# Kernel optimization log

Hardware: AMD Instinct MI355X
Metric: run time of the kernel (lower is better)

## Reference

```python
import jax, jax.numpy as jnp
import numpy as np

VOCAB = 32000
EMBED = 256
HIDDEN = 512
BATCH = 32
MAXLEN = 128


def setup_inputs() -> dict:
    key = jax.random.key(0)
    ks = jax.random.split(key, 8)
    s = 0.02
    return {
        "text": jax.random.randint(ks[0], (BATCH, MAXLEN), 0, VOCAB, dtype=jnp.int64),
        "embed": jax.random.normal(ks[1], (VOCAB, EMBED), dtype=jnp.float32) * s,
        "W_ih": jax.random.normal(ks[2], (4 * HIDDEN, EMBED), dtype=jnp.float32) * s,
        "W_hh": jax.random.normal(ks[3], (4 * HIDDEN, HIDDEN), dtype=jnp.float32) * s,
        "b_ih": jax.random.normal(ks[4], (4 * HIDDEN,), dtype=jnp.float32) * s,
        "b_hh": jax.random.normal(ks[5], (4 * HIDDEN,), dtype=jnp.float32) * s,
        "W_fc": jax.random.normal(ks[6], (VOCAB, HIDDEN), dtype=jnp.float32) * s,
        "b_fc": jax.random.normal(ks[7], (VOCAB,), dtype=jnp.float32) * s,
    }


def reference(text, embed, W_ih, W_hh, b_ih, b_hh, W_fc, b_fc):
    B, T = text.shape
    H = W_hh.shape[1]

    def step(carry, _):
        h, c, tok = carry
        x = embed[tok]                                  # [B, E] gather
        gates = x @ W_ih.T + b_ih + h @ W_hh.T + b_hh   # [B, 4H]
        i, f, g, o = jnp.split(gates, 4, axis=-1)       # PyTorch LSTMCell gate order
        i = jax.nn.sigmoid(i)
        f = jax.nn.sigmoid(f)
        g = jnp.tanh(g)
        o = jax.nn.sigmoid(o)
        c = f * c + i * g
        h = o * jnp.tanh(c)
        logits = h @ W_fc.T + b_fc                      # [B, V]
        tok = jnp.argmax(logits, axis=1)                # greedy feedback
        return (h, c, tok), logits

    # initial prediction = zeros[B,1] -> argmax = token 0; hidden=None -> zeros
    init = (
        jnp.zeros((B, H), dtype=embed.dtype),
        jnp.zeros((B, H), dtype=embed.dtype),
        jnp.zeros((B,), dtype=jnp.int32),
    )
    _, logits = jax.lax.scan(step, init, None, length=T)  # [T, B, V]
    return jnp.transpose(logits, (1, 0, 2))               # [B, T, V]
```

## Files before the change

### kernel.cpp

```cpp
#include <hip/hip_runtime.h>
#include <hip/hip_bf16.h>
#include <math.h>

#define VOCAB  32000
#define EMBED  256
#define HIDDEN 512
#define BATCH  32
#define MAXLEN 128
#define NCAND  250

typedef __attribute__((ext_vector_type(8))) short bf16x8;
typedef __attribute__((ext_vector_type(8))) unsigned short ushort8;
typedef __attribute__((ext_vector_type(4))) float f32x4;

#define WS_C_OFF     0
#define WS_HHI_OFF   65536
#define WS_HLO_OFF   131072
#define WS_CAND_OFF  196608
#define WS_WHI_OFF   260608
#define WS_WLO_OFF   33028608
#define WS_ZERO_BYTES 196608

__device__ __forceinline__ unsigned int f32_ordered_key(float f) {
    unsigned int b = __float_as_uint(f);
    return (b & 0x80000000u) ? ~b : (b | 0x80000000u);
}
__device__ __forceinline__ unsigned short f2bf(float x) {
    __hip_bfloat16 h = __float2bfloat16(x);
    return *reinterpret_cast<unsigned short*>(&h);
}
__device__ __forceinline__ float bf2f(unsigned short u) {
    __hip_bfloat16 h = *reinterpret_cast<__hip_bfloat16*>(&u);
    return __bfloat162float(h);
}

__global__ __launch_bounds__(256) void split_w_kernel(
    const float* __restrict__ W, unsigned short* __restrict__ hi,
    unsigned short* __restrict__ lo, int n4)
{
    const int stride = gridDim.x * blockDim.x;
    for (int i = blockIdx.x * blockDim.x + threadIdx.x; i < n4; i += stride) {
        f32x4 w = ((const f32x4*)W)[i];
        ushort4 hv, lv;
        #pragma unroll
        for (int j = 0; j < 4; ++j) {
            float x = w[j];
            unsigned short hb = f2bf(x);
            ((unsigned short*)&hv)[j] = hb;
            ((unsigned short*)&lv)[j] = f2bf(x - bf2f(hb));
        }
        ((ushort4*)hi)[i] = hv;
        ((ushort4*)lo)[i] = lv;
    }
}

__global__ __launch_bounds__(256) void lstm_step_kernel(
    const float* __restrict__ embed,
    const float* __restrict__ W_ih, const float* __restrict__ W_hh,
    const float* __restrict__ b_ih, const float* __restrict__ b_hh,
    const unsigned long long* __restrict__ cand,
    const unsigned short* __restrict__ hhi_prev, const unsigned short* __restrict__ hlo_prev,
    unsigned short* __restrict__ hhi_next, unsigned short* __restrict__ hlo_next,
    float* __restrict__ c_buf, int t)
{
    __shared__ float x_t[EMBED][33];
    __shared__ float h_t[HIDDEN][33];
    __shared__ int   tok_s[BATCH];
    __shared__ unsigned long long credl[8][BATCH];
    __shared__ float part[2][4][BATCH][4];
    __shared__ float gate_s[2][4][BATCH];

    const int tid = threadIdx.x;

    if (t > 0) {
        const int rb = tid & 31, seg = tid >> 5;
        unsigned long long m = 0ull;
        for (int i = seg; i < NCAND; i += 8) {
            unsigned long long e = cand[(size_t)i * BATCH + rb];
            if (e > m) m = e;
        }
        credl[seg][rb] = m;
        __syncthreads();
        if (tid < BATCH) {
            unsigned long long mm = credl[0][tid];
            #pragma unroll
            for (int ss = 1; ss < 8; ++ss) if (credl[ss][tid] > mm) mm = credl[ss][tid];
            tok_s[tid] = (int)(~(unsigned int)(mm & 0xFFFFFFFFull));
        }
    } else {
        if (tid < BATCH) tok_s[tid] = 0;
    }
    __syncthreads();

    {
        const int sb = tid >> 3, slot = tid & 7;
        const float* er = embed + (size_t)tok_s[sb] * EMBED;
        #pragma unroll
        for (int i = 0; i < 8; ++i) {
            int e4 = i * 8 + slot;
            float4 v = ((const float4*)er)[e4];
            int e = e4 * 4;
            x_t[e + 0][sb] = v.x; x_t[e + 1][sb] = v.y;
            x_t[e + 2][sb] = v.z; x_t[e + 3][sb] = v.w;
        }
        const ushort8* hr = (const ushort8*)(hhi_prev + (size_t)sb * HIDDEN);
        const ushort8* lr = (const ushort8*)(hlo_prev + (size_t)sb * HIDDEN);
        #pragma unroll
        for (int i = 0; i < 8; ++i) {
            int u = i * 8 + slot;
            ushort8 hv = hr[u], lv = lr[u];
            #pragma unroll
            for (int e = 0; e < 8; ++e)
                h_t[u * 8 + e][sb] = bf2f((unsigned short)hv[e]) + bf2f((unsigned short)lv[e]);
        }
    }
    __syncthreads();

    const int b  = tid & 31;
    const int s  = (tid >> 5) & 3;
    const int jp = tid >> 7;
    const int j  = blockIdx.x * 2 + jp;

    float a0 = 0.f, a1 = 0.f, a2 = 0.f, a3 = 0.f;
    float d0 = 0.f, d1 = 0.f, d2 = 0.f, d3 = 0.f;

    {
        const float4* w0 = (const float4*)(W_ih + (size_t)j * EMBED) + s * 16;
        const float4* w1 = (const float4*)(W_ih + (size_t)(HIDDEN + j) * EMBED) + s * 16;
        const float4* w2 = (const float4*)(W_ih + (size_t)(2 * HIDDEN + j) * EMBED) + s * 16;
        const float4* w3 = (const float4*)(W_ih + (size_t)(3 * HIDDEN + j) * EMBED) + s * 16;
        #pragma unroll 4
        for (int g = 0; g < 16; ++g) {
            float4 W0 = w0[g], W1 = w1[g], W2 = w2[g], W3 = w3[g];
            int e = s * 64 + g * 4;
            float x0 = x_t[e + 0][b], x1 = x_t[e + 1][b], x2 = x_t[e + 2][b], x3 = x_t[e + 3][b];
            a0 = fmaf(W0.x, x0, a0); d0 = fmaf(W0.y, x1, d0); a0 = fmaf(W0.z, x2, a0); d0 = fmaf(W0.w, x3, d0);
            a1 = fmaf(W1.x, x0, a1); d1 = fmaf(W1.y, x1, d1); a1 = fmaf(W1.z, x2, a1); d1 = fmaf(W1.w, x3, d1);
            a2 = fmaf(W2.x, x0, a2); d2 = fmaf(W2.y, x1, d2); a2 = fmaf(W2.z, x2, a2); d2 = fmaf(W2.w, x3, d2);
            a3 = fmaf(W3.x, x0, a3); d3 = fmaf(W3.y, x1, d3); a3 = fmaf(W3.z, x2, a3); d3 = fmaf(W3.w, x3, d3);
        }
    }
    {
        const float4* w0 = (const float4*)(W_hh + (size_t)j * HIDDEN) + s * 32;
        const float4* w1 = (const float4*)(W_hh + (size_t)(HIDDEN + j) * HIDDEN) + s * 32;
        const float4* w2 = (const float4*)(W_hh + (size_t)(2 * HIDDEN + j) * HIDDEN) + s * 32;
        const float4* w3 = (const float4*)(W_hh + (size_t)(3 * HIDDEN + j) * HIDDEN) + s * 32;
        #pragma unroll 4
        for (int g = 0; g < 32; ++g) {
            float4 W0 = w0[g], W1 = w1[g], W2 = w2[g], W3 = w3[g];
            int k = s * 128 + g * 4;
            float x0 = h_t[k + 0][b], x1 = h_t[k + 1][b], x2 = h_t[k + 2][b], x3 = h_t[k + 3][b];
            a0 = fmaf(W0.x, x0, a0); d0 = fmaf(W0.y, x1, d0); a0 = fmaf(W0.z, x2, a0); d0 = fmaf(W0.w, x3, d0);
            a1 = fmaf(W1.x, x0, a1); d1 = fmaf(W1.y, x1, d1); a1 = fmaf(W1.z, x2, a1); d1 = fmaf(W1.w, x3, d1);
            a2 = fmaf(W2.x, x0, a2); d2 = fmaf(W2.y, x1, d2); a2 = fmaf(W2.z, x2, a2); d2 = fmaf(W2.w, x3, d2);
            a3 = fmaf(W3.x, x0, a3); d3 = fmaf(W3.y, x1, d3); a3 = fmaf(W3.z, x2, a3); d3 = fmaf(W3.w, x3, d3);
        }
    }
    part[jp][s][b][0] = a0 + d0;
    part[jp][s][b][1] = a1 + d1;
    part[jp][s][b][2] = a2 + d2;
    part[jp][s][b][3] = a3 + d3;
    __syncthreads();

    {
        const int gb = tid & 31, gate = (tid >> 5) & 3, gjp = tid >> 7;
        const int jj = blockIdx.x * 2 + gjp;
        float g = part[gjp][0][gb][gate] + part[gjp][1][gb][gate]
                + part[gjp][2][gb][gate] + part[gjp][3][gb][gate];
        g += b_ih[gate * HIDDEN + jj] + b_hh[gate * HIDDEN + jj];
        gate_s[gjp][gate][gb] = (gate == 2) ? tanhf(g) : 1.f / (1.f + expf(-g));
    }
    __syncthreads();

    if (tid < 64) {
        const int cb = tid & 31, cjp = tid >> 5;
        const int jj = blockIdx.x * 2 + cjp;
        const float iv = gate_s[cjp][0][cb], fv = gate_s[cjp][1][cb];
        const float gv = gate_s[cjp][2][cb], ov = gate_s[cjp][3][cb];
        const size_t off = (size_t)cb * HIDDEN + jj;
        float cn = fv * c_buf[off] + iv * gv;
        c_buf[off] = cn;
        float hv = ov * tanhf(cn);
        unsigned short hh = f2bf(hv);
        hhi_next[off] = hh;
        hlo_next[off] = f2bf(hv - bf2f(hh));
    }
}

#define MFMA(a, b, c) __builtin_amdgcn_mfma_f32_16x16x32_bf16((a), (b), (c), 0, 0, 0)
#define HPTR(arr, bb, cc) \
    ((const bf16x8*)((const char*)(arr) + ((((bb) * 1024) + (kg * 16) + (cc) * 64) ^ ((((bb) & 7)) << 4))))

__global__ __launch_bounds__(512) void logits_mfma_kernel(
    const unsigned short* __restrict__ Whi, const unsigned short* __restrict__ Wlo,
    const unsigned short* __restrict__ hhi, const unsigned short* __restrict__ hlo,
    const float* __restrict__ b_fc, float* __restrict__ out,
    unsigned long long* __restrict__ cand, int t)
{
    __shared__ unsigned short hs_hi[BATCH * HIDDEN];
    __shared__ unsigned short hs_lo[BATCH * HIDDEN];
    __shared__ unsigned long long red[8][BATCH];

    const int tid = threadIdx.x;

    #pragma unroll
    for (int i = 0; i < 8; ++i) {
        int u   = i * 512 + tid;
        int arr = u >> 11;
        int b   = (u >> 6) & 31;
        int k16 = u & 63;
        const unsigned short* src = (arr ? hlo : hhi) + (size_t)b * HIDDEN + k16 * 8;
        int4 v = *(const int4*)src;
        char* dst = (char*)(arr ? hs_lo : hs_hi) + ((b * 1024 + k16 * 16) ^ ((b & 7) << 4));
        *(int4*)dst = v;
    }
    __syncthreads();

    const int w    = tid >> 6;
    const int lane = tid & 63;
    const int row  = lane & 15;
    const int kg   = lane >> 4;
    const int vwave = blockIdx.x * 128 + w * 16;

    const unsigned short* wh = Whi + (size_t)(vwave + row) * HIDDEN + kg * 8;
    const unsigned short* wl = Wlo + (size_t)(vwave + row) * HIDDEN + kg * 8;

    f32x4 acc0 = {0.f, 0.f, 0.f, 0.f};
    f32x4 acc1 = {0.f, 0.f, 0.f, 0.f};

    bf16x8 awh = *(const bf16x8*)(wh);
    bf16x8 awl = *(const bf16x8*)(wl);
    #pragma unroll
    for (int c = 0; c < 15; ++c) {
        bf16x8 nwh = *(const bf16x8*)(wh + (c + 1) * 32);
        bf16x8 nwl = *(const bf16x8*)(wl + (c + 1) * 32);
        bf16x8 hh0 = *HPTR(hs_hi, row, c),      hh1 = *HPTR(hs_hi, row + 16, c);
        bf16x8 hl0 = *HPTR(hs_lo, row, c),      hl1 = *HPTR(hs_lo, row + 16, c);
        acc0 = MFMA(awh, hh0, acc0); acc1 = MFMA(awh, hh1, acc1);
        acc0 = MFMA(awl, hh0, acc0); acc1 = MFMA(awl, hh1, acc1);
        acc0 = MFMA(awh, hl0, acc0); acc1 = MFMA(awh, hl1, acc1);
        awh = nwh; awl = nwl;
    }
    {
        const int c = 15;
        bf16x8 hh0 = *HPTR(hs_hi, row, c),      hh1 = *HPTR(hs_hi, row + 16, c);
        bf16x8 hl0 = *HPTR(hs_lo, row, c),      hl1 = *HPTR(hs_lo, row + 16, c);
        acc0 = MFMA(awh, hh0, acc0); acc1 = MFMA(awh, hh1, acc1);
        acc0 = MFMA(awl, hh0, acc0); acc1 = MFMA(awl, hh1, acc1);
        acc0 = MFMA(awh, hl0, acc0); acc1 = MFMA(awh, hl1, acc1);
    }

    const int v4 = vwave + kg * 4;
    f32x4 bias = *(const f32x4*)(b_fc + v4);
    f32x4 st0, st1;
    unsigned long long best0 = 0ull, best1 = 0ull;
    #pragma unroll
    for (int jj = 0; jj < 4; ++jj) {
        st0[jj] = acc0[jj] + bias[jj];
        st1[jj] = acc1[jj] + bias[jj];
        unsigned long long e0 = ((unsigned long long)f32_ordered_key(st0[jj]) << 32)
                              | (unsigned long long)(~(unsigned int)(v4 + jj));
        unsigned long long e1 = ((unsigned long long)f32_ordered_key(st1[jj]) << 32)
                              | (unsigned long long)(~(unsigned int)(v4 + jj));
        if (e0 > best0) best0 = e0;
        if (e1 > best1) best1 = e1;
    }
    *(f32x4*)(out + ((size_t)row * MAXLEN + t) * VOCAB + v4)        = st0;
    *(f32x4*)(out + ((size_t)(row + 16) * MAXLEN + t) * VOCAB + v4) = st1;

    #pragma unroll
    for (int sft = 16; sft <= 32; sft <<= 1) {
        unsigned long long o0 = __shfl_xor(best0, sft, 64);
        unsigned long long o1 = __shfl_xor(best1, sft, 64);
        if (o0 > best0) best0 = o0;
        if (o1 > best1) best1 = o1;
    }
    if (kg == 0) { red[w][row] = best0; red[w][row + 16] = best1; }
    __syncthreads();
    if (tid < BATCH) {
        unsigned long long m = red[0][tid];
        #pragma unroll
        for (int ww = 1; ww < 8; ++ww) if (red[ww][tid] > m) m = red[ww][tid];
        cand[(size_t)blockIdx.x * BATCH + tid] = m;
    }
}

extern "C" void kernel_launch(void* const* d_in, const int* in_sizes, int n_in,
                              void* d_out, int out_size, void* d_ws, size_t ws_size,
                              hipStream_t stream) {
    const float* embed = (const float*)d_in[1];
    const float* W_ih  = (const float*)d_in[2];
    const float* W_hh  = (const float*)d_in[3];
    const float* b_ih  = (const float*)d_in[4];
    const float* b_hh  = (const float*)d_in[5];
    const float* W_fc  = (const float*)d_in[6];
    const float* b_fc  = (const float*)d_in[7];
    float* out = (float*)d_out;

    char* ws = (char*)d_ws;
    float* c_buf = (float*)(ws + WS_C_OFF);
    unsigned short* h_hi = (unsigned short*)(ws + WS_HHI_OFF);
    unsigned short* h_lo = (unsigned short*)(ws + WS_HLO_OFF);
    unsigned long long* cand = (unsigned long long*)(ws + WS_CAND_OFF);
    unsigned short* W_hi = (unsigned short*)(ws + WS_WHI_OFF);
    unsigned short* W_lo = (unsigned short*)(ws + WS_WLO_OFF);

    hipMemsetAsync(d_ws, 0, WS_ZERO_BYTES, stream);
    split_w_kernel<<<2048, 256, 0, stream>>>(W_fc, W_hi, W_lo, VOCAB * HIDDEN / 4);

    for (int t = 0; t < MAXLEN; ++t) {
        const int p = t & 1;
        unsigned short* hhi_prev = h_hi + (size_t)p * BATCH * HIDDEN;
        unsigned short* hlo_prev = h_lo + (size_t)p * BATCH * HIDDEN;
        unsigned short* hhi_next = h_hi + (size_t)(p ^ 1) * BATCH * HIDDEN;
        unsigned short* hlo_next = h_lo + (size_t)(p ^ 1) * BATCH * HIDDEN;
        lstm_step_kernel<<<256, 256, 0, stream>>>(
            embed, W_ih, W_hh, b_ih, b_hh, cand,
            hhi_prev, hlo_prev, hhi_next, hlo_next, c_buf, t);
        logits_mfma_kernel<<<NCAND, 512, 0, stream>>>(
            W_hi, W_lo, hhi_next, hlo_next, b_fc, out, cand, t);
    }
}
```

Baseline: 4.648 ms.

## Split logits K dimension across wave pairs and double candidate blocks

Each block of the logits kernel now covers 64 vocab rows instead of 128, and each 16-row tile is split into two K halves handled by separate waves, with partial sums combined through shared memory. The launch therefore has twice as many blocks (500 candidates), which is meant to fill more CUs and shorten each wave's serial MFMA chain. Even and odd accumulators are kept separate to break MFMA dependency chains, and output stores use nontemporal hints. The cost is an extra shared-memory reduction and barrier per block, the same h tile staged into LDS by twice as many blocks, and more candidates to reduce afterwards.

```diff
diff --git a/kernel.cpp b/kernel.cpp
--- a/kernel.cpp
+++ b/kernel.cpp
@@ -7,7 +7,8 @@
 #define HIDDEN 512
 #define BATCH  32
 #define MAXLEN 128
-#define NCAND  250
+#define NCAND  500
+#define VB     64
 
 typedef __attribute__((ext_vector_type(8))) short bf16x8;
 typedef __attribute__((ext_vector_type(8))) unsigned short ushort8;
@@ -17,8 +18,8 @@
 #define WS_HHI_OFF   65536
 #define WS_HLO_OFF   131072
 #define WS_CAND_OFF  196608
-#define WS_WHI_OFF   260608
-#define WS_WLO_OFF   33028608
+#define WS_WHI_OFF   324608
+#define WS_WLO_OFF   33092608
 #define WS_ZERO_BYTES 196608
 
 __device__ __forceinline__ unsigned int f32_ordered_key(float f) {
@@ -199,7 +200,8 @@
 {
     __shared__ unsigned short hs_hi[BATCH * HIDDEN];
     __shared__ unsigned short hs_lo[BATCH * HIDDEN];
-    __shared__ unsigned long long red[8][BATCH];
+    __shared__ f32x4 partial[4][64][2];
+    __shared__ unsigned long long red[4][BATCH];
 
     const int tid = threadIdx.x;
 
@@ -216,71 +218,89 @@
     }
     __syncthreads();
 
-    const int w    = tid >> 6;
-    const int lane = tid & 63;
-    const int row  = lane & 15;
-    const int kg   = lane >> 4;
-    const int vwave = blockIdx.x * 128 + w * 16;
-
-    const unsigned short* wh = Whi + (size_t)(vwave + row) * HIDDEN + kg * 8;
-    const unsigned short* wl = Wlo + (size_t)(vwave + row) * HIDDEN + kg * 8;
-
-    f32x4 acc0 = {0.f, 0.f, 0.f, 0.f};
-    f32x4 acc1 = {0.f, 0.f, 0.f, 0.f};
+    const int w     = tid >> 6;
+    const int lane  = tid & 63;
+    const int vtile = w >> 1;
+    const int khalf = w & 1;
+    const int row   = lane & 15;
+    const int kg    = lane >> 4;
+    const int vbase = blockIdx.x * VB + vtile * 16;
+
+    const unsigned short* wh = Whi + (size_t)(vbase + row) * HIDDEN + khalf * 256 + kg * 8;
+    const unsigned short* wl = Wlo + (size_t)(vbase + row) * HIDDEN + khalf * 256 + kg * 8;
+
+    f32x4 acc0e = {0.f,0.f,0.f,0.f}, acc0o = {0.f,0.f,0.f,0.f};
+    f32x4 acc1e = {0.f,0.f,0.f,0.f}, acc1o = {0.f,0.f,0.f,0.f};
 
     bf16x8 awh = *(const bf16x8*)(wh);
     bf16x8 awl = *(const bf16x8*)(wl);
     #pragma unroll
-    for (int c = 0; c < 15; ++c) {
-        bf16x8 nwh = *(const bf16x8*)(wh + (c + 1) * 32);
-        bf16x8 nwl = *(const bf16x8*)(wl + (c + 1) * 32);
-        bf16x8 hh0 = *HPTR(hs_hi, row, c),      hh1 = *HPTR(hs_hi, row + 16, c);
-        bf16x8 hl0 = *HPTR(hs_lo, row, c),      hl1 = *HPTR(hs_lo, row + 16, c);
-        acc0 = MFMA(awh, hh0, acc0); acc1 = MFMA(awh, hh1, acc1);
-        acc0 = MFMA(awl, hh0, acc0); acc1 = MFMA(awl, hh1, acc1);
-        acc0 = MFMA(awh, hl0, acc0); acc1 = MFMA(awh, hl1, acc1);
+    for (int c = 0; c < 8; ++c) {
+        const int cg = khalf * 8 + c;
+        bf16x8 nwh = awh, nwl = awl;
+        if (c < 7) {
+            nwh = *(const bf16x8*)(wh + (c + 1) * 32);
+            nwl = *(const bf16x8*)(wl + (c + 1) * 32);
+        }
+        bf16x8 hh0 = *HPTR(hs_hi, row, cg),      hh1 = *HPTR(hs_hi, row + 16, cg);
+        bf16x8 hl0 = *HPTR(hs_lo, row, cg),      hl1 = *HPTR(hs_lo, row + 16, cg);
+        if (c & 1) {
+            acc0o = MFMA(awh, hh0, acc0o); acc1o = MFMA(awh, hh1, acc1o);
+            acc0o = MFMA(awl, hh0, acc0o); acc1o = MFMA(awl, hh1, acc1o);
+            acc0o = MFMA(awh, hl0, acc0o); acc1o = MFMA(awh, hl1, acc1o);
+        } else {
+            acc0e = MFMA(awh, hh0, acc0e); acc1e = MFMA(awh, hh1, acc1e);
+            acc0e = MFMA(awl, hh0, acc0e); acc1e = MFMA(awl, hh1, acc1e);
+            acc0e = MFMA(awh, hl0, acc0e); acc1e = MFMA(awh, hl1, acc1e);
+        }
         awh = nwh; awl = nwl;
     }
-    {
-        const int c = 15;
-        bf16x8 hh0 = *HPTR(hs_hi, row, c),      hh1 = *HPTR(hs_hi, row + 16, c);
-        bf16x8 hl0 = *HPTR(hs_lo, row, c),      hl1 = *HPTR(hs_lo, row + 16, c);
-        acc0 = MFMA(awh, hh0, acc0); acc1 = MFMA(awh, hh1, acc1);
-        acc0 = MFMA(awl, hh0, acc0); acc1 = MFMA(awl, hh1, acc1);
-        acc0 = MFMA(awh, hl0, acc0); acc1 = MFMA(awh, hl1, acc1);
-    }
-
-    const int v4 = vwave + kg * 4;
-    f32x4 bias = *(const f32x4*)(b_fc + v4);
-    f32x4 st0, st1;
-    unsigned long long best0 = 0ull, best1 = 0ull;
-    #pragma unroll
-    for (int jj = 0; jj < 4; ++jj) {
-        st0[jj] = acc0[jj] + bias[jj];
-        st1[jj] = acc1[jj] + bias[jj];
-        unsigned long long e0 = ((unsigned long long)f32_ordered_key(st0[jj]) << 32)
-                              | (unsigned long long)(~(unsigned int)(v4 + jj));
-        unsigned long long e1 = ((unsigned long long)f32_ordered_key(st1[jj]) << 32)
-                              | (unsigned long long)(~(unsigned int)(v4 + jj));
-        if (e0 > best0) best0 = e0;
-        if (e1 > best1) best1 = e1;
-    }
-    *(f32x4*)(out + ((size_t)row * MAXLEN + t) * VOCAB + v4)        = st0;
-    *(f32x4*)(out + ((size_t)(row + 16) * MAXLEN + t) * VOCAB + v4) = st1;
-
-    #pragma unroll
-    for (int sft = 16; sft <= 32; sft <<= 1) {
-        unsigned long long o0 = __shfl_xor(best0, sft, 64);
-        unsigned long long o1 = __shfl_xor(best1, sft, 64);
-        if (o0 > best0) best0 = o0;
-        if (o1 > best1) best1 = o1;
-    }
-    if (kg == 0) { red[w][row] = best0; red[w][row + 16] = best1; }
+
+    f32x4 acc0 = acc0e + acc0o;
+    f32x4 acc1 = acc1e + acc1o;
+
+    if (khalf == 1) {
+        partial[vtile][lane][0] = acc0;
+        partial[vtile][lane][1] = acc1;
+    }
+    __syncthreads();
+
+    if (khalf == 0) {
+        acc0 += partial[vtile][lane][0];
+        acc1 += partial[vtile][lane][1];
+
+        const int v4 = vbase + kg * 4;
+        f32x4 bias = *(const f32x4*)(b_fc + v4);
+        f32x4 st0, st1;
+        unsigned long long best0 = 0ull, best1 = 0ull;
+        #pragma unroll
+        for (int jj = 0; jj < 4; ++jj) {
+            st0[jj] = acc0[jj] + bias[jj];
+            st1[jj] = acc1[jj] + bias[jj];
+            unsigned long long e0 = ((unsigned long long)f32_ordered_key(st0[jj]) << 32)
+                                  | (unsigned long long)(~(unsigned int)(v4 + jj));
+            unsigned long long e1 = ((unsigned long long)f32_ordered_key(st1[jj]) << 32)
+                                  | (unsigned long long)(~(unsigned int)(v4 + jj));
+            if (e0 > best0) best0 = e0;
+            if (e1 > best1) best1 = e1;
+        }
+        __builtin_nontemporal_store(st0, (f32x4*)(out + ((size_t)row * MAXLEN + t) * VOCAB + v4));
+        __builtin_nontemporal_store(st1, (f32x4*)(out + ((size_t)(row + 16) * MAXLEN + t) * VOCAB + v4));
+
+        #pragma unroll
+        for (int sft = 16; sft <= 32; sft <<= 1) {
+            unsigned long long o0 = __shfl_xor(best0, sft, 64);
+            unsigned long long o1 = __shfl_xor(best1, sft, 64);
+            if (o0 > best0) best0 = o0;
+            if (o1 > best1) best1 = o1;
+        }
+        if (kg == 0) { red[vtile][row] = best0; red[vtile][row + 16] = best1; }
+    }
     __syncthreads();
     if (tid < BATCH) {
         unsigned long long m = red[0][tid];
         #pragma unroll
-        for (int ww = 1; ww < 8; ++ww) if (red[ww][tid] > m) m = red[ww][tid];
+        for (int vv = 1; vv < 4; ++vv) if (red[vv][tid] > m) m = red[vv][tid];
         cand[(size_t)blockIdx.x * BATCH + tid] = m;
     }
 }
```

Measured after the change: 5.542 ms. 1.19x slower.
